# Kernel tuning notes

Hardware: AMD Instinct MI355X
Metric: run time of the kernel (lower is better)

Reference implementation:

```python
import jax, jax.numpy as jnp
import numpy as np

# Plan (mirrors pytorch_ffa's plan.steps rows)
PLAN = [{"dsfactor": 1.0, "bins_min": 128, "bins_max": 132, "tsamp": 0.000064}]

B, C, T = 4, 2, 2097152


def _linear_resize(x, out_len):
    # F.interpolate(mode='linear', align_corners=False) equivalent (no antialias)
    in_len = x.shape[-1]
    if out_len == in_len:
        return x
    scale = in_len / out_len
    src = (jnp.arange(out_len, dtype=jnp.float32) + 0.5) * scale - 0.5
    src = jnp.clip(src, 0.0, in_len - 1)
    lo = jnp.floor(src).astype(jnp.int32)
    hi = jnp.minimum(lo + 1, in_len - 1)
    w = src - lo.astype(jnp.float32)
    return x[..., lo] * (1.0 - w) + x[..., hi] * w


def _groupshiftadd(x, n_row_group):
    # x: [B, C, G, n_row_group, nCol]; vectorized over the row-group loop:
    # y[i] = x[i//2] + roll(x[i//2 + half], (i+1)//2)
    n_col = x.shape[-1]
    half = n_row_group // 2
    i = np.arange(n_row_group)
    iA = i // 2
    iB = iA + half
    Bs = (i + 1) // 2
    # roll by Bs[i] along last axis == gather at (j - Bs[i]) mod nCol
    col = (np.arange(n_col)[None, :] - Bs[:, None]) % n_col  # [n_row_group, nCol]
    xA = x[:, :, :, iA, :]
    xB = jnp.take_along_axis(x[:, :, :, iB, :], jnp.asarray(col)[None, None, None, :, :], axis=4)
    return xA + xB


def _ffa(x):
    # x: [B, C, R, bins] with R a power of two; log2(R) butterfly stages
    b, c, R, n_col = x.shape
    nstage = int(np.log2(R))
    for stage in range(1, nstage + 1):
        g = 2 ** stage
        x = _groupshiftadd(x.reshape(b, c, R // g, g, n_col), g)
        x = x.reshape(b, c, R, n_col)
    return x


def _calc_snr(profiles, added_rows, std_dev):
    # torch.median returns the lower median (sorted index (n-1)//2)
    bins = profiles.shape[3]
    mx = profiles.max(axis=3)
    med = jnp.sort(profiles, axis=3)[..., (bins - 1) // 2]
    return (mx - med) / std_dev[:, :, None] / np.sqrt(profiles.shape[2] - added_rows)


def reference(x):
    std_dev = jnp.std(x, axis=2, ddof=1)  # torch .std() is unbiased
    outs = []
    periods = []
    for step in PLAN:
        out_len = int(x.shape[2] // step["dsfactor"])  # floor(N * 1/scale)
        down = _linear_resize(x, out_len)
        for bins in range(step["bins_min"], step["bins_max"]):
            trunc = down.shape[2] % bins
            p = down[:, :, :down.shape[2] - trunc] if trunc else down
            r = p.reshape(p.shape[0], p.shape[1], -1, bins)
            rows = r.shape[2]
            target = 1 << int(np.ceil(np.log2(rows)))
            added = target - rows
            if added:
                r = jnp.pad(r, ((0, 0), (0, 0), (0, added), (0, 0)))
            ffa_out = _ffa(r)
            outs.append(_calc_snr(ffa_out, added, std_dev))
            p0 = step["tsamp"] * bins
            p1 = step["tsamp"] * (bins + 1)
            periods.append(np.linspace(p0, p1, target))
    return jnp.asarray(np.concatenate(periods), dtype=jnp.float32), jnp.concatenate(outs, axis=2)


def setup_inputs() -> dict:
    key = jax.random.key(0)
    x = jax.random.normal(key, (B, C, T), dtype=jnp.float32)
    return {"x": x}
```

## Files before the change

kernel.cpp:

```cpp
#include <hip/hip_runtime.h>
#include <hip/hip_fp16.h>
#include <math.h>


typedef unsigned int u32;

#define T_LEN   2097152
#define RTOT    16384
#define YSTR    70
#define B_BUF_DW (128 * YSTR)
#define PP_LDS_BYTES (2 * B_BUF_DW * 4)

#define WS_PART_OFF 0
#define WS_STD_OFF  32768
#define WS_Y_OFF    33024
#define WS_NEEDED   (33024 + (size_t)8 * RTOT * YSTR * 4)

#define HINF2 0x7C007C00u
#define NINF2 0xFC00FC00u

__device__ __forceinline__ u32 alnp(u32 lo, u32 hi) { return (lo >> 16) | (hi << 16); }
__device__ __forceinline__ __half2 asH2(u32 v) { union { u32 u; __half2 h; } x; x.u = v; return x.h; }
__device__ __forceinline__ u32 asU32(__half2 h) { union { u32 u; __half2 h2; } x; x.h2 = h; return x.u; }
__device__ __forceinline__ u32 hmin2u(u32 a, u32 b) {
  u32 r; asm("v_pk_min_f16 %0, %1, %2" : "=v"(r) : "v"(a), "v"(b)); return r;
}
__device__ __forceinline__ u32 hmax2u(u32 a, u32 b) {
  u32 r; asm("v_pk_max_f16 %0, %1, %2" : "=v"(r) : "v"(a), "v"(b)); return r;
}

__global__ void k_periods(float* __restrict__ out) {
  int i = blockIdx.x * 256 + threadIdx.x;
  int bi = i >> 14, j = i & 16383;
  double tsamp = 6.4e-05;
  double p0 = tsamp * (double)(128 + bi);
  double p1 = tsamp * (double)(129 + bi);
  double step = (p1 - p0) / 16383.0;
  double v = (j == 16383) ? p1 : (p0 + (double)j * step);
  out[i] = (float)v;
}

__global__ void k_std_final(const double* __restrict__ part, float* __restrict__ stddev) {
  int t = threadIdx.x;
  if (t < 8) {
    double s = 0.0, s2 = 0.0;
    for (int G = 0; G < 128; ++G) {
      s  += part[(t * 128 + G) * 2];
      s2 += part[(t * 128 + G) * 2 + 1];
    }
    double N = (double)T_LEN;
    double var = (s2 - s * s / N) / (N - 1.0);
    stddev[t] = (float)sqrt(var);
  }
}

__device__ __forceinline__ void pair16_col(const u32* r0p, const u32* r1p,
                                           const u32* r2p, const u32* r3p,
                                           int c0, int s1p, int s2p, int s3p,
                                           int ncol, u32 outw[4]) {
  u32 a = r0p[c0 >> 1];
  int q1 = c0 - s1p; if (q1 < 0) q1 += ncol;
  int q2 = c0 - s2p; if (q2 < 0) q2 += ncol;
  int q3 = c0 - s3p; if (q3 < 0) q3 += ncol;
  int b1 = q1 >> 1, o1 = q1 & 1;
  int b2 = q2 >> 1, o2 = q2 & 1;
  int b3 = q3 >> 1, o3 = q3 & 1;
  u32 d10 = r1p[b1], d11 = r1p[b1 + 1];
  u32 d20 = r2p[b2], d21 = r2p[b2 + 1], d22 = r2p[b2 + 2];
  u32 d30 = r3p[b3], d31 = r3p[b3 + 1], d32 = r3p[b3 + 2];
  u32 a1m = alnp(d10, d11);
  u32 a2a = alnp(d20, d21), a2b = alnp(d21, d22);
  u32 a3a = alnp(d30, d31), a3b = alnp(d31, d32);
  u32 V1[2] = { o1 ? a1m : d10,  o1 ? d11 : a1m };
  u32 V2[3] = { o2 ? a2a : d20,  o2 ? d21 : a2a,  o2 ? a2b : d21 };
  u32 V3[4] = { o3 ? a3a : d30,  o3 ? d31 : a3a,  o3 ? a3b : d31,  o3 ? d32 : a3b };
#pragma unroll
  for (int o = 0; o < 4; ++o) {
    int d1 = 1 - (o >> 1);
    int d2 = 2 - ((o + 1) >> 1);
    int d3 = 3 - o;
    __half2 rr = __hadd2(__hadd2(asH2(a), asH2(V1[d1])),
                         __hadd2(asH2(V2[d2]), asH2(V3[d3])));
    outw[o] = asU32(rr);
  }
}

template <int NCOL, int ST>
__device__ __forceinline__ void ffa_pair16(const u32* src, u32* dst, int rextra) {
  int t = threadIdx.x;
  int Q = t >> 5;
  int l = t & 31;
  constexpr int g = 1 << ST;
  int q = Q & ((g >> 1) - 1);
  int B = (Q >> (ST - 1)) << (ST + 1);
  int e1 = (rextra << (ST - 1)) % NCOL;
  int e2m = (rextra << ST) % NCOL;
  int s1 = q + e1; if (s1 >= NCOL) s1 -= NCOL;
  int s2 = 2 * q + e2m; if (s2 >= NCOL) s2 -= NCOL;
  int s3 = s1 + s2; if (s3 >= NCOL) s3 -= NCOL;
  int s1p = s1 + 1; if (s1p >= NCOL) s1p -= NCOL;
  int s2p = s2 + 2; if (s2p >= NCOL) s2p -= NCOL;
  int s3p = s3 + 3; if (s3p >= NCOL) s3p -= NCOL;
  const u32* r0p = src + (size_t)(B + q) * YSTR;
  const u32* r1p = r0p + (size_t)(g >> 1) * YSTR;
  const u32* r2p = r0p + (size_t)g * YSTR;
  const u32* r3p = r2p + (size_t)(g >> 1) * YSTR;

  __syncthreads();

  u32 outm[2][4];
  pair16_col(r0p, r1p, r2p, r3p, 2 * l,      s1p, s2p, s3p, NCOL, outm[0]);
  pair16_col(r0p, r1p, r2p, r3p, 2 * l + 64, s1p, s2p, s3p, NCOL, outm[1]);
  u32 outt[4];
  bool tact0 = (NCOL > 128) && (l == 0);
  bool tact1 = (NCOL == 131) && (l == 1);
  if (tact0) pair16_col(r0p, r1p, r2p, r3p, 128, s1p, s2p, s3p, NCOL, outt);
  if (tact1) pair16_col(r0p, r1p, r2p, r3p, 130, s1p, s2p, s3p, NCOL, outt);

#pragma unroll
  for (int p = 0; p < 2; ++p)
#pragma unroll
    for (int o = 0; o < 4; ++o)
      dst[(size_t)(B + 4 * q + o) * YSTR + l + 32 * p] = outm[p][o];
  if (l < 3) {
#pragma unroll
    for (int o = 0; o < 4; ++o) {
      __half* hr = (__half*)(dst + (size_t)(B + 4 * q + o) * YSTR);
      __half2 hv = asH2(outm[0][o]);
      hr[NCOL + 2 * l]     = __low2half(hv);
      hr[NCOL + 2 * l + 1] = __high2half(hv);
    }
  }
  if (tact0) {
#pragma unroll
    for (int o = 0; o < 4; ++o) {
      __half* hr = (__half*)(dst + (size_t)(B + 4 * q + o) * YSTR);
      __half2 hv = asH2(outt[o]);
      hr[128] = __low2half(hv);
      if (NCOL > 129) hr[129] = __high2half(hv);
    }
  }
  if (tact1) {
#pragma unroll
    for (int o = 0; o < 4; ++o) {
      __half* hr = (__half*)(dst + (size_t)(B + 4 * q + o) * YSTR);
      hr[130] = __low2half(asH2(outt[o]));
    }
  }
}

template <int NCOL, bool STD>
__global__ __launch_bounds__(1024, 8) void k_passA(const float* __restrict__ x,
                                                   u32* __restrict__ y,
                                                   double* __restrict__ part,
                                                   int rows_actual) {
  extern __shared__ u32 lds16[];
  __shared__ double sm2[32];
  u32* buf0 = lds16;
  u32* buf1 = lds16 + B_BUF_DW;
  int G = blockIdx.x, bc = blockIdx.y, t = threadIdx.x;

  const float* src = x + (size_t)bc * T_LEN + (size_t)G * 128 * NCOL;
  double ds = 0.0, ds2 = 0.0;

  if constexpr (NCOL == 128) {
    const float4* src4 = (const float4*)src;
#pragma unroll
    for (int i = 0; i < 4; ++i) {
      int idx = t + i * 1024;
      float4 v = src4[idx];
      if (STD) {
        ds  += (double)(v.x + v.y + v.z + v.w);
        ds2 += (double)(v.x * v.x + v.y * v.y + v.z * v.z + v.w * v.w);
      }
      int k = idx >> 5, c = (idx & 31) * 4;
      uint2 pk;
      pk.x = asU32(__floats2half2_rn(v.x, v.y));
      pk.y = asU32(__floats2half2_rn(v.z, v.w));
      *(uint2*)(buf0 + k * YSTR + (c >> 1)) = pk;
      if (c < 8) *(uint2*)(buf0 + k * YSTR + 64 + (c >> 1)) = pk;
    }
    (void)rows_actual;
  } else {
    int rowlim = rows_actual - G * 128;
    int lim = rowlim * NCOL;
    __half* hb = (__half*)buf0;
    constexpr int NF2 = 128 * NCOL / 2;
#pragma unroll
    for (int i = 0; i < (NF2 + 1023) / 1024; ++i) {
      int e2 = t + i * 1024;
      if (e2 < NF2) {
        int e = e2 * 2;
        float2 v = make_float2(0.f, 0.f);
        if (e + 1 < lim) {
          v = *(const float2*)(src + e);
        } else if (e < lim) {
          v.x = src[e];
        }
        int k = e / NCOL, c = e % NCOL;
        __half h0 = __float2half_rn(v.x), h1 = __float2half_rn(v.y);
        hb[k * 140 + c] = h0;
        if (c < 6) hb[k * 140 + NCOL + c] = h0;
        int k2 = k, c2 = c + 1;
        if (c2 == NCOL) { c2 = 0; ++k2; }
        hb[k2 * 140 + c2] = h1;
        if (c2 < 6) hb[k2 * 140 + NCOL + c2] = h1;
      }
    }
  }
  if (STD) {
    for (int off = 32; off > 0; off >>= 1) {
      ds  += __shfl_down(ds, off);
      ds2 += __shfl_down(ds2, off);
    }
    int wid = t >> 6, lane = t & 63;
    if (lane == 0) { sm2[wid] = ds; sm2[16 + wid] = ds2; }
  }

  ffa_pair16<NCOL, 1>(buf0, buf1, 0);
  ffa_pair16<NCOL, 3>(buf1, buf0, 0);
  ffa_pair16<NCOL, 5>(buf0, buf1, 0);
  __syncthreads();

  {
    int p = t >> 4, hh = t & 15;
    const u32* ra = buf1 + (size_t)p * YSTR;
    const u32* rb = buf1 + (size_t)(p + 64) * YSTR;
    u32* dstE = y + ((size_t)bc * RTOT + (size_t)(2 * p) * 128 + G) * YSTR;
    u32* dstO = dstE + (size_t)128 * YSTR;
#pragma unroll
    for (int i = 0; i < 4; ++i) {
      int i0 = hh + 16 * i;
      int j0 = 2 * i0;
      u32 a = ra[i0];
      int qe = j0 - p;  if (qe < 0) qe += NCOL;
      int qo = qe - 1;  if (qo < 0) qo += NCOL;
      u32 be, bo;
      { int bb = qe >> 1; u32 e0 = rb[bb], e1v = rb[bb + 1];
        be = (qe & 1) ? alnp(e0, e1v) : e0; }
      { int bb = qo >> 1; u32 e0 = rb[bb], e1v = rb[bb + 1];
        bo = (qo & 1) ? alnp(e0, e1v) : e0; }
      u32 ve = asU32(__hadd2(asH2(a), asH2(be)));
      u32 vo = asU32(__hadd2(asH2(a), asH2(bo)));
      dstE[i0] = ve;
      dstO[i0] = vo;
      if (i == 0 && hh < 3) {
        __half* hE = (__half*)dstE;
        __half* hO = (__half*)dstO;
        __half2 hve = asH2(ve), hvo = asH2(vo);
        hE[NCOL + j0]     = __low2half(hve);
        hE[NCOL + j0 + 1] = __high2half(hve);
        hO[NCOL + j0]     = __low2half(hvo);
        hO[NCOL + j0 + 1] = __high2half(hvo);
      }
    }
    if (NCOL > 128 && hh == 0) {
      int j0 = 128;
      u32 a = ra[64];
      int qe = j0 - p;
      int qo = qe - 1;
      u32 be, bo;
      { int bb = qe >> 1; u32 e0 = rb[bb], e1v = rb[bb + 1];
        be = (qe & 1) ? alnp(e0, e1v) : e0; }
      { int bb = qo >> 1; u32 e0 = rb[bb], e1v = rb[bb + 1];
        bo = (qo & 1) ? alnp(e0, e1v) : e0; }
      u32 ve = asU32(__hadd2(asH2(a), asH2(be)));
      u32 vo = asU32(__hadd2(asH2(a), asH2(bo)));
      if (NCOL > 129) {
        dstE[64] = ve; dstO[64] = vo;
      } else {
        ((__half*)dstE)[128] = __low2half(asH2(ve));
        ((__half*)dstO)[128] = __low2half(asH2(vo));
      }
    }
    if (NCOL == 131 && hh == 1) {
      int j0 = 130;
      u32 a = ra[65];
      int qe = j0 - p;
      int qo = qe - 1;
      u32 be, bo;
      { int bb = qe >> 1; u32 e0 = rb[bb], e1v = rb[bb + 1];
        be = (qe & 1) ? alnp(e0, e1v) : e0; }
      { int bb = qo >> 1; u32 e0 = rb[bb], e1v = rb[bb + 1];
        bo = (qo & 1) ? alnp(e0, e1v) : e0; }
      ((__half*)dstE)[130] = __low2half(__hadd2(asH2(a), asH2(be)));
      ((__half*)dstO)[130] = __low2half(__hadd2(asH2(a), asH2(bo)));
    }
  }

  if (STD && t == 0) {
    double s = 0.0, s2 = 0.0;
#pragma unroll
    for (int w = 0; w < 16; ++w) { s += sm2[w]; s2 += sm2[16 + w]; }
    part[(bc * 128 + G) * 2]     = s;
    part[(bc * 128 + G) * 2 + 1] = s2;
  }
}

template <int NCOL>
__global__ __launch_bounds__(1024, 8) void k_passB(const u32* __restrict__ y,
                                                   const float* __restrict__ stddev,
                                                   float* __restrict__ out,
                                                   int added, int bins_idx) {
  extern __shared__ u32 lds16[];
  u32* buf0 = lds16;
  u32* buf1 = lds16 + B_BUF_DW;
  int r = blockIdx.x, bc = blockIdx.y, t = threadIdx.x;

  const uint4* src4 = (const uint4*)(y + ((size_t)bc * RTOT + (size_t)r * 128) * YSTR);
#pragma unroll
  for (int i = 0; i < 3; ++i) {
    int idx = t + i * 1024;
    if (idx < 2240) *(uint4*)(buf0 + idx * 4) = src4[idx];
  }

  ffa_pair16<NCOL, 1>(buf0, buf1, r);
  ffa_pair16<NCOL, 3>(buf1, buf0, r);
  ffa_pair16<NCOL, 5>(buf0, buf1, r);
  __syncthreads();

  int u = t >> 3, h = t & 7;
  int p = u >> 1;
  int extra = (r << 6) % NCOL;
  int s = p + extra; if (s >= NCOL) s -= NCOL;
  s += (u & 1);      if (s >= NCOL) s -= NCOL;
  const u32* ra = buf1 + (size_t)p * YSTR;
  const u32* rb = buf1 + (size_t)(p + 64) * YSTR;
  constexpr int NCHUNK = (NCOL + 3) / 4;
  constexpr int NCK = (NCHUNK + 7) / 8;
  u32 valp[NCK * 2];
  u32 mn2 = HINF2, mx2 = NINF2;
#pragma unroll
  for (int i = 0; i < NCK; ++i) {
    if (NCOL <= 128 || i < 4) {
      int ch = h + 8 * i;
      int j0 = ch * 4;
      uint2 aa = *(const uint2*)(ra + 2 * ch);
      int q0 = j0 - s; if (q0 < 0) q0 += NCOL;
      int bb = q0 >> 1, ob = q0 & 1;
      u32 e0 = rb[bb], e1 = rb[bb + 1], e2 = rb[bb + 2];
      u32 blo = ob ? alnp(e0, e1) : e0;
      u32 bhi = ob ? alnp(e1, e2) : e1;
      u32 v0 = asU32(__hadd2(asH2(aa.x), asH2(blo)));
      u32 v1 = asU32(__hadd2(asH2(aa.y), asH2(bhi)));
      valp[2 * i]     = v0;
      valp[2 * i + 1] = v1;
      mn2 = hmin2u(hmin2u(mn2, v0), v1);
      mx2 = hmax2u(hmax2u(mx2, v0), v1);
    } else {
      if (h == 0) {
        constexpr int j0 = 128;
        uint2 aa = *(const uint2*)(ra + 64);
        int q0 = j0 - s; if (q0 < 0) q0 += NCOL;
        int bb = q0 >> 1, ob = q0 & 1;
        u32 e0 = rb[bb], e1 = rb[bb + 1], e2 = rb[bb + 2];
        u32 blo = ob ? alnp(e0, e1) : e0;
        u32 bhi = ob ? alnp(e1, e2) : e1;
        u32 v0 = asU32(__hadd2(asH2(aa.x), asH2(blo)));
        u32 v1 = asU32(__hadd2(asH2(aa.y), asH2(bhi)));
        u32 v0mn, v1mn, v0mx, v1mx;
        if (NCOL == 129) {
          v0mn = (v0 & 0xFFFFu) | 0x7C000000u; v0mx = (v0 & 0xFFFFu) | 0xFC000000u;
          v1mn = HINF2;                        v1mx = NINF2;
        } else if (NCOL == 130) {
          v0mn = v0;                           v0mx = v0;
          v1mn = HINF2;                        v1mx = NINF2;
        } else {
          v0mn = v0;                           v0mx = v0;
          v1mn = (v1 & 0xFFFFu) | 0x7C000000u; v1mx = (v1 & 0xFFFFu) | 0xFC000000u;
        }
        valp[2 * i]     = v0mn;
        valp[2 * i + 1] = v1mn;
        mn2 = hmin2u(hmin2u(mn2, v0mn), v1mn);
        mx2 = hmax2u(hmax2u(mx2, v0mx), v1mx);
      } else {
        valp[2 * i]     = HINF2;
        valp[2 * i + 1] = HINF2;
      }
    }
  }
#pragma unroll
  for (int off = 1; off < 8; off <<= 1) {
    mn2 = hmin2u(mn2, (u32)__shfl_xor((int)mn2, off));
    mx2 = hmax2u(mx2, (u32)__shfl_xor((int)mx2, off));
  }
  float mn = fminf(__low2float(asH2(mn2)), __high2float(asH2(mn2)));
  float mx = fmaxf(__low2float(asH2(mx2)), __high2float(asH2(mx2)));

  u32* hrow = buf0 + (size_t)u * 68;
  {
    uint4 z = make_uint4(0u, 0u, 0u, 0u);
    *(uint4*)(hrow + h * 8)     = z;
    *(uint4*)(hrow + h * 8 + 4) = z;
  }
  float rng = mx - mn;
  float scale = 128.0f / fmaxf(rng, 1e-30f);
#pragma unroll
  for (int i = 0; i < NCK * 2; ++i) {
    __half2 hv = asH2(valp[i]);
    float f0 = __low2float(hv), f1 = __high2float(hv);
    int b0 = min((int)((f0 - mn) * scale), 127);
    int b1 = min((int)((f1 - mn) * scale), 127);
    atomicAdd(&hrow[b0 >> 1], 1u << ((b0 & 1) * 16));
    atomicAdd(&hrow[b1 >> 1], 1u << ((b1 & 1) * 16));
  }
  int cnt[16];
  {
    uint4 c0v = *(const uint4*)(hrow + h * 8);
    uint4 c1v = *(const uint4*)(hrow + h * 8 + 4);
    u32 w[8] = {c0v.x, c0v.y, c0v.z, c0v.w, c1v.x, c1v.y, c1v.z, c1v.w};
#pragma unroll
    for (int m = 0; m < 8; ++m) {
      cnt[2 * m]     = (int)(w[m] & 0xFFFFu);
      cnt[2 * m + 1] = (int)(w[m] >> 16);
    }
  }
  int local = 0;
#pragma unroll
  for (int i = 0; i < 16; ++i) local += cnt[i];
  int incl = local, tmp;
  tmp = __shfl_up(incl, 1, 8); if (h >= 1) incl += tmp;
  tmp = __shfl_up(incl, 2, 8); if (h >= 2) incl += tmp;
  tmp = __shfl_up(incl, 4, 8); if (h >= 4) incl += tmp;
  int excl = incl - local;
  constexpr int TR = ((NCOL - 1) >> 1) + 1;
  int cum = excl, cross = 0;
#pragma unroll
  for (int i = 0; i < 16; ++i) {
    cum += cnt[i];
    cross += (cum < TR) ? 1 : 0;
  }
  int bcand = (excl < TR && TR <= incl) ? (h * 16 + cross) : (1 << 30);
#pragma unroll
  for (int off = 1; off < 8; off <<= 1)
    bcand = min(bcand, __shfl_xor(bcand, off));

  float med = mn + ((float)bcand + 0.5f) * rng * (1.0f / 128.0f);
  float denom = stddev[bc] * sqrtf((float)(RTOT - added));
  float snr = (mx - med) / denom;
  if (h == 0)
    out[65536 + (size_t)bc * 65536 + (size_t)bins_idx * RTOT + r * 128 + u] = snr;
}

extern "C" void kernel_launch(void* const* d_in, const int* in_sizes, int n_in,
                              void* d_out, int out_size, void* d_ws, size_t ws_size,
                              hipStream_t stream) {
  const float* x = (const float*)d_in[0];
  float* out = (float*)d_out;
  char* ws = (char*)d_ws;
  if (ws_size < WS_NEEDED) return;

  double* part   = (double*)(ws + WS_PART_OFF);
  float*  stddev = (float*) (ws + WS_STD_OFF);
  u32*    y      = (u32*)   (ws + WS_Y_OFF);

  (void)hipFuncSetAttribute((const void*)k_passA<128, true>,  hipFuncAttributeMaxDynamicSharedMemorySize, PP_LDS_BYTES);
  (void)hipFuncSetAttribute((const void*)k_passA<129, false>, hipFuncAttributeMaxDynamicSharedMemorySize, PP_LDS_BYTES);
  (void)hipFuncSetAttribute((const void*)k_passA<130, false>, hipFuncAttributeMaxDynamicSharedMemorySize, PP_LDS_BYTES);
  (void)hipFuncSetAttribute((const void*)k_passA<131, false>, hipFuncAttributeMaxDynamicSharedMemorySize, PP_LDS_BYTES);
  (void)hipFuncSetAttribute((const void*)k_passB<128>, hipFuncAttributeMaxDynamicSharedMemorySize, PP_LDS_BYTES);
  (void)hipFuncSetAttribute((const void*)k_passB<129>, hipFuncAttributeMaxDynamicSharedMemorySize, PP_LDS_BYTES);
  (void)hipFuncSetAttribute((const void*)k_passB<130>, hipFuncAttributeMaxDynamicSharedMemorySize, PP_LDS_BYTES);
  (void)hipFuncSetAttribute((const void*)k_passB<131>, hipFuncAttributeMaxDynamicSharedMemorySize, PP_LDS_BYTES);

  k_periods<<<256, 256, 0, stream>>>(out);

  k_passA<128, true><<<dim3(128, 8), 1024, PP_LDS_BYTES, stream>>>(x, y, part, 16384);
  k_std_final<<<1, 64, 0, stream>>>(part, stddev);
  k_passB<128><<<dim3(128, 8), 1024, PP_LDS_BYTES, stream>>>(y, stddev, out, 0, 0);
  k_passA<129, false><<<dim3(128, 8), 1024, PP_LDS_BYTES, stream>>>(x, y, part, 16256);
  k_passB<129><<<dim3(128, 8), 1024, PP_LDS_BYTES, stream>>>(y, stddev, out, 128, 1);
  k_passA<130, false><<<dim3(128, 8), 1024, PP_LDS_BYTES, stream>>>(x, y, part, 16131);
  k_passB<130><<<dim3(128, 8), 1024, PP_LDS_BYTES, stream>>>(y, stddev, out, 253, 2);
  k_passA<131, false><<<dim3(128, 8), 1024, PP_LDS_BYTES, stream>>>(x, y, part, 16008);
  k_passB<131><<<dim3(128, 8), 1024, PP_LDS_BYTES, stream>>>(y, stddev, out, 376, 3);
}
```

Baseline: 265.9 us.

## Merge per-bin pass kernels into two launches and fold stddev into passB

```diff
diff --git a/kernel.cpp b/kernel.cpp
--- a/kernel.cpp
+++ b/kernel.cpp
@@ -10,11 +10,12 @@
 #define YSTR    70
 #define B_BUF_DW (128 * YSTR)
 #define PP_LDS_BYTES (2 * B_BUF_DW * 4)
+#define YBIN_DW ((size_t)8 * RTOT * YSTR)
 
 #define WS_PART_OFF 0
-#define WS_STD_OFF  32768
 #define WS_Y_OFF    33024
-#define WS_NEEDED   (33024 + (size_t)8 * RTOT * YSTR * 4)
+#define WS_SERIAL_NEEDED  (33024 + YBIN_DW * 4)
+#define WS_MERGED_NEEDED  (33024 + 4 * YBIN_DW * 4)
 
 #define HINF2 0x7C007C00u
 #define NINF2 0xFC00FC00u
@@ -38,20 +39,6 @@
   double step = (p1 - p0) / 16383.0;
   double v = (j == 16383) ? p1 : (p0 + (double)j * step);
   out[i] = (float)v;
-}
-
-__global__ void k_std_final(const double* __restrict__ part, float* __restrict__ stddev) {
-  int t = threadIdx.x;
-  if (t < 8) {
-    double s = 0.0, s2 = 0.0;
-    for (int G = 0; G < 128; ++G) {
-      s  += part[(t * 128 + G) * 2];
-      s2 += part[(t * 128 + G) * 2 + 1];
-    }
-    double N = (double)T_LEN;
-    double var = (s2 - s * s / N) / (N - 1.0);
-    stddev[t] = (float)sqrt(var);
-  }
 }
 
 __device__ __forceinline__ void pair16_col(const u32* r0p, const u32* r1p,
@@ -85,7 +72,7 @@
   }
 }
 
-template <int NCOL, int ST>
+template <int NCOL, int ST, bool BAR>
 __device__ __forceinline__ void ffa_pair16(const u32* src, u32* dst, int rextra) {
   int t = threadIdx.x;
   int Q = t >> 5;
@@ -106,7 +93,7 @@
   const u32* r2p = r0p + (size_t)g * YSTR;
   const u32* r3p = r2p + (size_t)(g >> 1) * YSTR;
 
-  __syncthreads();
+  if constexpr (BAR) __syncthreads();
 
   u32 outm[2][4];
   pair16_col(r0p, r1p, r2p, r3p, 2 * l,      s1p, s2p, s3p, NCOL, outm[0]);
@@ -150,16 +137,13 @@
 }
 
 template <int NCOL, bool STD>
-__global__ __launch_bounds__(1024, 8) void k_passA(const float* __restrict__ x,
-                                                   u32* __restrict__ y,
-                                                   double* __restrict__ part,
-                                                   int rows_actual) {
-  extern __shared__ u32 lds16[];
-  __shared__ double sm2[32];
-  u32* buf0 = lds16;
-  u32* buf1 = lds16 + B_BUF_DW;
+__device__ __forceinline__ void passA_body(const float* __restrict__ x,
+                                           u32* __restrict__ y,
+                                           double* __restrict__ part,
+                                           int rows_actual,
+                                           u32* buf0, u32* buf1, double* sm2) {
   int G = blockIdx.x, bc = blockIdx.y, t = threadIdx.x;
-
+  int w = t >> 6, lane = t & 63;
   const float* src = x + (size_t)bc * T_LEN + (size_t)G * 128 * NCOL;
   double ds = 0.0, ds2 = 0.0;
 
@@ -167,7 +151,7 @@
     const float4* src4 = (const float4*)src;
 #pragma unroll
     for (int i = 0; i < 4; ++i) {
-      int idx = t + i * 1024;
+      int idx = w * 256 + lane + 64 * i;
       float4 v = src4[idx];
       if (STD) {
         ds  += (double)(v.x + v.y + v.z + v.w);
@@ -185,11 +169,11 @@
     int rowlim = rows_actual - G * 128;
     int lim = rowlim * NCOL;
     __half* hb = (__half*)buf0;
-    constexpr int NF2 = 128 * NCOL / 2;
-#pragma unroll
-    for (int i = 0; i < (NF2 + 1023) / 1024; ++i) {
-      int e2 = t + i * 1024;
-      if (e2 < NF2) {
+    int base2 = 4 * NCOL * w;
+#pragma unroll
+    for (int i = 0; i < 9; ++i) {
+      int e2 = base2 + lane + 64 * i;
+      if (e2 < base2 + 4 * NCOL) {
         int e = e2 * 2;
         float2 v = make_float2(0.f, 0.f);
         if (e + 1 < lim) {
@@ -213,13 +197,12 @@
       ds  += __shfl_down(ds, off);
       ds2 += __shfl_down(ds2, off);
     }
-    int wid = t >> 6, lane = t & 63;
-    if (lane == 0) { sm2[wid] = ds; sm2[16 + wid] = ds2; }
-  }
-
-  ffa_pair16<NCOL, 1>(buf0, buf1, 0);
-  ffa_pair16<NCOL, 3>(buf1, buf0, 0);
-  ffa_pair16<NCOL, 5>(buf0, buf1, 0);
+    if (lane == 0) { sm2[w] = ds; sm2[16 + w] = ds2; }
+  }
+
+  ffa_pair16<NCOL, 1, false>(buf0, buf1, 0);
+  ffa_pair16<NCOL, 3, true >(buf1, buf0, 0);
+  ffa_pair16<NCOL, 5, true >(buf0, buf1, 0);
   __syncthreads();
 
   {
@@ -291,32 +274,45 @@
   if (STD && t == 0) {
     double s = 0.0, s2 = 0.0;
 #pragma unroll
-    for (int w = 0; w < 16; ++w) { s += sm2[w]; s2 += sm2[16 + w]; }
+    for (int ww = 0; ww < 16; ++ww) { s += sm2[ww]; s2 += sm2[16 + ww]; }
     part[(bc * 128 + G) * 2]     = s;
     part[(bc * 128 + G) * 2 + 1] = s2;
   }
 }
 
 template <int NCOL>
-__global__ __launch_bounds__(1024, 8) void k_passB(const u32* __restrict__ y,
-                                                   const float* __restrict__ stddev,
-                                                   float* __restrict__ out,
-                                                   int added, int bins_idx) {
-  extern __shared__ u32 lds16[];
-  u32* buf0 = lds16;
-  u32* buf1 = lds16 + B_BUF_DW;
+__device__ __forceinline__ void passB_body(const u32* __restrict__ y,
+                                           const double* __restrict__ part,
+                                           float* __restrict__ out,
+                                           int added, int bins_idx,
+                                           u32* buf0, u32* buf1, float* s_denom) {
   int r = blockIdx.x, bc = blockIdx.y, t = threadIdx.x;
+  int w = t >> 6, lane = t & 63;
+
+  if (t < 64) {
+    double s  = part[(bc * 128 + t) * 2]     + part[(bc * 128 + t + 64) * 2];
+    double s2 = part[(bc * 128 + t) * 2 + 1] + part[(bc * 128 + t + 64) * 2 + 1];
+    for (int off = 32; off > 0; off >>= 1) {
+      s  += __shfl_down(s, off);
+      s2 += __shfl_down(s2, off);
+    }
+    if (t == 0) {
+      double N = (double)T_LEN;
+      double var = (s2 - s * s / N) / (N - 1.0);
+      *s_denom = (float)(sqrt(var) * sqrt((double)(RTOT - added)));
+    }
+  }
 
   const uint4* src4 = (const uint4*)(y + ((size_t)bc * RTOT + (size_t)r * 128) * YSTR);
 #pragma unroll
   for (int i = 0; i < 3; ++i) {
-    int idx = t + i * 1024;
-    if (idx < 2240) *(uint4*)(buf0 + idx * 4) = src4[idx];
-  }
-
-  ffa_pair16<NCOL, 1>(buf0, buf1, r);
-  ffa_pair16<NCOL, 3>(buf1, buf0, r);
-  ffa_pair16<NCOL, 5>(buf0, buf1, r);
+    int idx = lane + 64 * i;
+    if (idx < 140) *(uint4*)(buf0 + (w * 140 + idx) * 4) = src4[w * 140 + idx];
+  }
+
+  ffa_pair16<NCOL, 1, false>(buf0, buf1, r);
+  ffa_pair16<NCOL, 3, true >(buf1, buf0, r);
+  ffa_pair16<NCOL, 5, true >(buf0, buf1, r);
   __syncthreads();
 
   int u = t >> 3, h = t & 7;
@@ -408,11 +404,11 @@
   {
     uint4 c0v = *(const uint4*)(hrow + h * 8);
     uint4 c1v = *(const uint4*)(hrow + h * 8 + 4);
-    u32 w[8] = {c0v.x, c0v.y, c0v.z, c0v.w, c1v.x, c1v.y, c1v.z, c1v.w};
+    u32 wv[8] = {c0v.x, c0v.y, c0v.z, c0v.w, c1v.x, c1v.y, c1v.z, c1v.w};
 #pragma unroll
     for (int m = 0; m < 8; ++m) {
-      cnt[2 * m]     = (int)(w[m] & 0xFFFFu);
-      cnt[2 * m + 1] = (int)(w[m] >> 16);
+      cnt[2 * m]     = (int)(wv[m] & 0xFFFFu);
+      cnt[2 * m + 1] = (int)(wv[m] >> 16);
     }
   }
   int local = 0;
@@ -436,10 +432,45 @@
     bcand = min(bcand, __shfl_xor(bcand, off));
 
   float med = mn + ((float)bcand + 0.5f) * rng * (1.0f / 128.0f);
-  float denom = stddev[bc] * sqrtf((float)(RTOT - added));
-  float snr = (mx - med) / denom;
+  float snr = (mx - med) / (*s_denom);
   if (h == 0)
     out[65536 + (size_t)bc * 65536 + (size_t)bins_idx * RTOT + r * 128 + u] = snr;
+}
+
+__global__ __launch_bounds__(1024, 8) void k_passA_m(const float* __restrict__ x,
+                                                     u32* __restrict__ y,
+                                                     double* __restrict__ part,
+                                                     int zbase, int multi) {
+  extern __shared__ u32 lds16[];
+  __shared__ double sm2[32];
+  u32* buf0 = lds16;
+  u32* buf1 = lds16 + B_BUF_DW;
+  int bi = blockIdx.z + zbase;
+  u32* yb = y + (multi ? (size_t)bi * YBIN_DW : 0);
+  switch (bi) {
+    case 0: passA_body<128, true >(x, yb, part, 16384, buf0, buf1, sm2); break;
+    case 1: passA_body<129, false>(x, yb, part, 16256, buf0, buf1, sm2); break;
+    case 2: passA_body<130, false>(x, yb, part, 16131, buf0, buf1, sm2); break;
+    default: passA_body<131, false>(x, yb, part, 16008, buf0, buf1, sm2); break;
+  }
+}
+
+__global__ __launch_bounds__(1024, 8) void k_passB_m(const u32* __restrict__ y,
+                                                     const double* __restrict__ part,
+                                                     float* __restrict__ out,
+                                                     int zbase, int multi) {
+  extern __shared__ u32 lds16[];
+  __shared__ float s_denom;
+  u32* buf0 = lds16;
+  u32* buf1 = lds16 + B_BUF_DW;
+  int bi = blockIdx.z + zbase;
+  const u32* yb = y + (multi ? (size_t)bi * YBIN_DW : 0);
+  switch (bi) {
+    case 0: passB_body<128>(yb, part, out, 0,   0, buf0, buf1, &s_denom); break;
+    case 1: passB_body<129>(yb, part, out, 128, 1, buf0, buf1, &s_denom); break;
+    case 2: passB_body<130>(yb, part, out, 253, 2, buf0, buf1, &s_denom); break;
+    default: passB_body<131>(yb, part, out, 376, 3, buf0, buf1, &s_denom); break;
+  }
 }
 
 extern "C" void kernel_launch(void* const* d_in, const int* in_sizes, int n_in,
@@ -448,30 +479,23 @@
   const float* x = (const float*)d_in[0];
   float* out = (float*)d_out;
   char* ws = (char*)d_ws;
-  if (ws_size < WS_NEEDED) return;
-
-  double* part   = (double*)(ws + WS_PART_OFF);
-  float*  stddev = (float*) (ws + WS_STD_OFF);
-  u32*    y      = (u32*)   (ws + WS_Y_OFF);
-
-  (void)hipFuncSetAttribute((const void*)k_passA<128, true>,  hipFuncAttributeMaxDynamicSharedMemorySize, PP_LDS_BYTES);
-  (void)hipFuncSetAttribute((const void*)k_passA<129, false>, hipFuncAttributeMaxDynamicSharedMemorySize, PP_LDS_BYTES);
-  (void)hipFuncSetAttribute((const void*)k_passA<130, false>, hipFuncAttributeMaxDynamicSharedMemorySize, PP_LDS_BYTES);
-  (void)hipFuncSetAttribute((const void*)k_passA<131, false>, hipFuncAttributeMaxDynamicSharedMemorySize, PP_LDS_BYTES);
-  (void)hipFuncSetAttribute((const void*)k_passB<128>, hipFuncAttributeMaxDynamicSharedMemorySize, PP_LDS_BYTES);
-  (void)hipFuncSetAttribute((const void*)k_passB<129>, hipFuncAttributeMaxDynamicSharedMemorySize, PP_LDS_BYTES);
-  (void)hipFuncSetAttribute((const void*)k_passB<130>, hipFuncAttributeMaxDynamicSharedMemorySize, PP_LDS_BYTES);
-  (void)hipFuncSetAttribute((const void*)k_passB<131>, hipFuncAttributeMaxDynamicSharedMemorySize, PP_LDS_BYTES);
+  if (ws_size < WS_SERIAL_NEEDED) return;
+
+  double* part = (double*)(ws + WS_PART_OFF);
+  u32*    y    = (u32*)   (ws + WS_Y_OFF);
+
+  (void)hipFuncSetAttribute((const void*)k_passA_m, hipFuncAttributeMaxDynamicSharedMemorySize, PP_LDS_BYTES);
+  (void)hipFuncSetAttribute((const void*)k_passB_m, hipFuncAttributeMaxDynamicSharedMemorySize, PP_LDS_BYTES);
 
   k_periods<<<256, 256, 0, stream>>>(out);
 
-  k_passA<128, true><<<dim3(128, 8), 1024, PP_LDS_BYTES, stream>>>(x, y, part, 16384);
-  k_std_final<<<1, 64, 0, stream>>>(part, stddev);
-  k_passB<128><<<dim3(128, 8), 1024, PP_LDS_BYTES, stream>>>(y, stddev, out, 0, 0);
-  k_passA<129, false><<<dim3(128, 8), 1024, PP_LDS_BYTES, stream>>>(x, y, part, 16256);
-  k_passB<129><<<dim3(128, 8), 1024, PP_LDS_BYTES, stream>>>(y, stddev, out, 128, 1);
-  k_passA<130, false><<<dim3(128, 8), 1024, PP_LDS_BYTES, stream>>>(x, y, part, 16131);
-  k_passB<130><<<dim3(128, 8), 1024, PP_LDS_BYTES, stream>>>(y, stddev, out, 253, 2);
-  k_passA<131, false><<<dim3(128, 8), 1024, PP_LDS_BYTES, stream>>>(x, y, part, 16008);
-  k_passB<131><<<dim3(128, 8), 1024, PP_LDS_BYTES, stream>>>(y, stddev, out, 376, 3);
-}
+  if (ws_size >= WS_MERGED_NEEDED) {
+    k_passA_m<<<dim3(128, 8, 4), 1024, PP_LDS_BYTES, stream>>>(x, y, part, 0, 1);
+    k_passB_m<<<dim3(128, 8, 4), 1024, PP_LDS_BYTES, stream>>>(y, part, out, 0, 1);
+  } else {
+    for (int bi = 0; bi < 4; ++bi) {
+      k_passA_m<<<dim3(128, 8, 1), 1024, PP_LDS_BYTES, stream>>>(x, y, part, bi, 0);
+      k_passB_m<<<dim3(128, 8, 1), 1024, PP_LDS_BYTES, stream>>>(y, part, out, bi, 0);
+    }
+  }
+}
```

Measured after the change: 283.5 us. 6.6% more time.
